# Kernel optimization log

Measured on AMD Instinct MI355X. Metric: run time of the kernel, lower is better.

## Reference

```python
import jax, jax.numpy as jnp
import numpy as np
from jax import lax

VOCAB, EMBED, HIDDEN, LAYERS = 32000, 256, 384, 6
B, S = 16, 512
SCALE = 0.05  # keep tanh out of saturation

def setup_inputs() -> dict:
    key = jax.random.key(0)
    ks = jax.random.split(key, 10)
    return {
        "x": jax.random.randint(ks[0], (B, S), 0, VOCAB),
        "emb": jax.random.normal(ks[1], (VOCAB, EMBED), jnp.float32) * SCALE,
        "W_ih0": jax.random.normal(ks[2], (HIDDEN, EMBED), jnp.float32) * SCALE,
        "W_ih": jax.random.normal(ks[3], (LAYERS - 1, HIDDEN, HIDDEN), jnp.float32) * SCALE,
        "W_hh": jax.random.normal(ks[4], (LAYERS, HIDDEN, HIDDEN), jnp.float32) * SCALE,
        "b_ih": jax.random.normal(ks[5], (LAYERS, HIDDEN), jnp.float32) * SCALE,
        "b_hh": jax.random.normal(ks[6], (LAYERS, HIDDEN), jnp.float32) * SCALE,
        "W_out": jax.random.normal(ks[7], (VOCAB, HIDDEN), jnp.float32) * SCALE,
        "b_out": jax.random.normal(ks[8], (VOCAB,), jnp.float32) * SCALE,
    }

def _rnn_layer(seq, Wi, Wh, bi, bh):
    # seq: [S, B, in_dim]; Elman: h_t = tanh(x_t Wi^T + bi + h_{t-1} Wh^T + bh)
    pre = jnp.einsum('sbi,hi->sbh', seq, Wi) + bi  # batched input projection
    h0 = jnp.zeros((seq.shape[1], Wh.shape[0]), seq.dtype)
    def step(h, p):
        h = jnp.tanh(p + h @ Wh.T + bh)
        return h, h
    _, out = lax.scan(step, h0, pre)
    return out  # [S, B, H]

def reference(x, emb, W_ih0, W_ih, W_hh, b_ih, b_hh, W_out, b_out):
    seq = jnp.swapaxes(emb[x], 0, 1)  # [S, B, E]
    for l in range(LAYERS):
        Wi = W_ih0 if l == 0 else W_ih[l - 1]
        seq = _rnn_layer(seq, Wi, W_hh[l], b_ih[l], b_hh[l])
        # inter-layer dropout: identity in eval mode
    out = jnp.swapaxes(seq, 0, 1)  # [B, S, H]
    return out @ W_out.T + b_out  # [B, S, V]
```

## Files before the change

kernel.cpp:

```cpp
#include <hip/hip_runtime.h>

typedef _Float16 f16;
typedef _Float16 f16x8 __attribute__((ext_vector_type(8)));
typedef _Float16 f16x4 __attribute__((ext_vector_type(4)));
typedef float f32x4 __attribute__((ext_vector_type(4)));

#define MFMA16(a, b, c) __builtin_amdgcn_mfma_f32_16x16x32_f16(a, b, c, 0, 0, 0)

#define CH 16
#define NCH 32
#define SLOT_H (CH * 24 * 64 * 4)

__device__ __forceinline__ float fast_tanh(float x) {
    float e = __builtin_amdgcn_exp2f(x * 2.885390081777927f);
    return 1.0f - 2.0f * __builtin_amdgcn_rcpf(e + 1.0f);
}

__device__ __forceinline__ void lds_barrier() {
    asm volatile("s_waitcnt lgkmcnt(0)" ::: "memory");
    __builtin_amdgcn_s_barrier();
    __builtin_amdgcn_sched_barrier(0);
}

__device__ __forceinline__ f16x8 ld_llc(const f16* p) {
    f16x8 v;
    asm volatile("global_load_dwordx4 %0, %1, off sc0 sc1" : "=v"(v) : "v"(p) : "memory");
    return v;
}
__device__ __forceinline__ f16x4 ld_llc_f16x4(const f16* p) {
    f16x4 v;
    asm volatile("global_load_dwordx2 %0, %1, off sc0 sc1" : "=v"(v) : "v"(p) : "memory");
    return v;
}

#define VWAIT4(N, x0, x1, x2, x3) \
    asm volatile("s_waitcnt vmcnt(" #N ")" : "+v"(x0), "+v"(x1), "+v"(x2), "+v"(x3))
#define VWAITH6(N, p0, p1, p2, p3, p4, p5) \
    asm volatile("s_waitcnt vmcnt(" #N ")" : "+v"(p0), "+v"(p1), "+v"(p2), "+v"(p3), "+v"(p4), "+v"(p5))

__device__ __forceinline__ void wait_flag(const int* f, int target) {
    if (threadIdx.x == 0) {
        while (__hip_atomic_load(f, __ATOMIC_RELAXED, __HIP_MEMORY_SCOPE_AGENT) < target) {
            __builtin_amdgcn_s_sleep(1);
        }
    }
    __syncthreads();
}
__device__ __forceinline__ void set_flag(int* f, int val) {
    __syncthreads();
    if (threadIdx.x == 0)
        __hip_atomic_store(f, val, __ATOMIC_RELEASE, __HIP_MEMORY_SCOPE_AGENT);
}

__global__ void cvt_kernel(const float* __restrict__ src, f16* __restrict__ dst, const int n4) {
    const int i = blockIdx.x * blockDim.x + threadIdx.x;
    if (i < n4) {
        const float4 v = ((const float4*)src)[i];
        f16x4 o = { (f16)v.x, (f16)v.y, (f16)v.z, (f16)v.w };
        *(f16x4*)(dst + (size_t)i * 4) = o;
    }
}

__global__ void bias_combine_kernel(const float* __restrict__ b_ih, const float* __restrict__ b_hh,
                                    float* __restrict__ bias_c) {
    const int i = blockIdx.x * blockDim.x + threadIdx.x;
    if (i < 6 * 384) bias_c[i] = b_ih[i] + b_hh[i];
}

__global__ void embed_kernel(const int* __restrict__ x, const float* __restrict__ emb,
                             f16* __restrict__ seq0) {
    const int token = blockIdx.x;
    const int s = token >> 4, b = token & 15;
    const int idx = x[b * 512 + s];
    const float4 v = ((const float4*)(emb + (size_t)idx * 256))[threadIdx.x];
    f16x4 o = { (f16)v.x, (f16)v.y, (f16)v.z, (f16)v.w };
    *(f16x4*)(seq0 + (size_t)token * 256 + threadIdx.x * 4) = o;
}

template<int NK>
__device__ __forceinline__ void a_role(const f16* __restrict__ in_seq,
                                       const f16* __restrict__ Wi,
                                       const float* __restrict__ bias,
                                       f16* __restrict__ preL,
                                       const int* flag_in, int* flag_pre, const int* flag_seq,
                                       const int L) {
    const int tid = threadIdx.x, lane = tid & 63, w = tid >> 6;
    const int lr = lane & 15, lq = lane >> 4;
    const int KIN = NK * 32;

    f16x8 WiF[6][NK];
#pragma unroll
    for (int i = 0; i < 6; ++i) {
        const f16* wrow = Wi + (size_t)((w * 6 + i) * 16 + lr) * KIN + lq * 8;
#pragma unroll
        for (int kk = 0; kk < NK; ++kk) WiF[i][kk] = *(const f16x8*)(wrow + kk * 32);
    }
    float bv[6];
#pragma unroll
    for (int i = 0; i < 6; ++i) bv[i] = bias[(w * 6 + i) * 16 + lr];

    for (int c = 0; c < NCH; ++c) {
        if (L > 0) wait_flag(flag_in, c + 1);
        if (c >= 4) wait_flag(flag_seq, c - 3);

        f16* slot = preL + (size_t)(c & 3) * SLOT_H;
#pragma unroll 1
        for (int sc = 0; sc < CH; ++sc) {
            const int t = c * CH + sc;
            f32x4 acc[6];
#pragma unroll
            for (int i = 0; i < 6; ++i) acc[i] = (f32x4){ bv[i], bv[i], bv[i], bv[i] };

            const f16* ar = in_seq + (size_t)(t * 16 + lr) * KIN + lq * 8;
            f16x8 a[NK];
#pragma unroll
            for (int kk = 0; kk < NK; ++kk) a[kk] = ld_llc(ar + kk * 32);
            if constexpr (NK == 12) {
                VWAIT4(8, a[0], a[1], a[2], a[3]);
#pragma unroll
                for (int kk = 0; kk < 4; ++kk)
#pragma unroll
                    for (int i = 0; i < 6; ++i) acc[i] = MFMA16(a[kk], WiF[i][kk], acc[i]);
                VWAIT4(4, a[4], a[5], a[6], a[7]);
#pragma unroll
                for (int kk = 4; kk < 8; ++kk)
#pragma unroll
                    for (int i = 0; i < 6; ++i) acc[i] = MFMA16(a[kk], WiF[i][kk], acc[i]);
                VWAIT4(0, a[8], a[9], a[10], a[11]);
#pragma unroll
                for (int kk = 8; kk < 12; ++kk)
#pragma unroll
                    for (int i = 0; i < 6; ++i) acc[i] = MFMA16(a[kk], WiF[i][kk], acc[i]);
            } else {
                VWAIT4(4, a[0], a[1], a[2], a[3]);
#pragma unroll
                for (int kk = 0; kk < 4; ++kk)
#pragma unroll
                    for (int i = 0; i < 6; ++i) acc[i] = MFMA16(a[kk], WiF[i][kk], acc[i]);
                VWAIT4(0, a[4], a[5], a[6], a[7]);
#pragma unroll
                for (int kk = 4; kk < 8; ++kk)
#pragma unroll
                    for (int i = 0; i < 6; ++i) acc[i] = MFMA16(a[kk], WiF[i][kk], acc[i]);
            }
#pragma unroll
            for (int i = 0; i < 6; ++i) {
                f16x4 ph = { (f16)acc[i][0], (f16)acc[i][1], (f16)acc[i][2], (f16)acc[i][3] };
                *(f16x4*)(slot + ((size_t)(sc * 24 + w * 6 + i) * 64 + lane) * 4) = ph;
            }
        }
        set_flag(flag_pre, c + 1);
    }
}

__device__ __forceinline__ void b_role(const f16* __restrict__ preL,
                                       const f16* __restrict__ Wh,
                                       f16* __restrict__ out_seq,
                                       const int* flag_pre, int* flag_seq,
                                       f16 (*hbuf)[16][392]) {
    const int tid = threadIdx.x, lane = tid & 63, w = tid >> 6;
    const int lr = lane & 15, lq = lane >> 4, kb = lq * 8;

    for (int i = tid; i < 2 * 16 * 392; i += 256) (&hbuf[0][0][0])[i] = (f16)0.0f;

    f16x8 WhF[6][12];
#pragma unroll
    for (int i = 0; i < 6; ++i) {
        const f16* wrow = Wh + (size_t)((w * 6 + i) * 16 + lr) * 384 + kb;
#pragma unroll
        for (int kk = 0; kk < 12; ++kk) WhF[i][kk] = *(const f16x8*)(wrow + kk * 32);
    }
    __syncthreads();

    const int crow = tid >> 4;
    const int ccol = (tid & 15) * 8;

    for (int c = 0; c < NCH; ++c) {
        wait_flag(flag_pre, c + 1);
        const f16* slot = preL + (size_t)(c & 3) * SLOT_H;

#pragma unroll 1
        for (int g = 0; g < CH / 4; ++g) {
            f16x4 pr[4][6];
#pragma unroll
            for (int s = 0; s < 4; ++s)
#pragma unroll
                for (int i = 0; i < 6; ++i)
                    pr[s][i] = ld_llc_f16x4(slot + ((size_t)((g * 4 + s) * 24 + w * 6 + i) * 64 + lane) * 4);
            VWAITH6(0, pr[0][0], pr[0][1], pr[0][2], pr[0][3], pr[0][4], pr[0][5]);
            VWAITH6(0, pr[1][0], pr[1][1], pr[1][2], pr[1][3], pr[1][4], pr[1][5]);
            VWAITH6(0, pr[2][0], pr[2][1], pr[2][2], pr[2][3], pr[2][4], pr[2][5]);
            VWAITH6(0, pr[3][0], pr[3][1], pr[3][2], pr[3][3], pr[3][4], pr[3][5]);

#pragma unroll
            for (int s4 = 0; s4 < 4; ++s4) {
                const int sc = g * 4 + s4;
                const int t = c * CH + sc;
                f32x4 acc[6];
#pragma unroll
                for (int i = 0; i < 6; ++i) acc[i] = (f32x4){ 0.f, 0.f, 0.f, 0.f };

                const f16* hb = &hbuf[sc & 1][0][0] + lr * 392 + kb;
#pragma unroll
                for (int kk = 0; kk < 12; ++kk) {
                    const f16x8 a = *(const f16x8*)(hb + kk * 32);
#pragma unroll
                    for (int i = 0; i < 6; ++i) acc[i] = MFMA16(a, WhF[i][kk], acc[i]);
                }

                f16* hn = &hbuf[(sc + 1) & 1][0][0];
#pragma unroll
                for (int i = 0; i < 6; ++i) {
                    const int n = (w * 6 + i) * 16 + lr;
#pragma unroll
                    for (int r = 0; r < 4; ++r) {
                        const float v = acc[i][r] + (float)pr[s4][i][r];
                        hn[(lq * 4 + r) * 392 + n] = (f16)fast_tanh(v);
                    }
                }
                lds_barrier();
                const f16* hs = &hbuf[(sc + 1) & 1][0][0] + crow * 392 + ccol;
                f16* og = out_seq + (size_t)(t * 16 + crow) * 384 + ccol;
#pragma unroll
                for (int p = 0; p < 3; ++p)
                    *(f16x8*)(og + p * 128) = *(const f16x8*)(hs + p * 128);
            }
        }
        set_flag(flag_seq, c + 1);
    }
}

__global__ __launch_bounds__(256, 1) void pipeline_kernel(
    const f16* __restrict__ seq0, const f16* __restrict__ Wi0,
    const f16* __restrict__ WiR, const f16* __restrict__ WhAll,
    const float* __restrict__ biasAll, f16* __restrict__ sA, f16* __restrict__ sB,
    f16* __restrict__ preRing, int* __restrict__ flags) {
    __shared__ f16 hbuf[2][16][392];
    const int bid = blockIdx.x;
    if (bid < 6) {
        const int L = bid;
        const f16* in_seq = (L == 0) ? seq0 : ((L & 1) ? sA : sB);
        const f16* Wi = (L == 0) ? Wi0 : (WiR + (size_t)(L - 1) * 384 * 384);
        f16* preL = preRing + (size_t)L * 4 * SLOT_H;
        if (L == 0)
            a_role<8>(in_seq, Wi, biasAll, preL, nullptr, flags + 8, flags + 0, 0);
        else
            a_role<12>(in_seq, Wi, biasAll + L * 384, preL, flags + (L - 1), flags + 8 + L, flags + L, L);
    } else {
        const int L = bid - 6;
        f16* outb = (L & 1) ? sB : sA;
        b_role(preRing + (size_t)L * 4 * SLOT_H, WhAll + (size_t)L * 384 * 384, outb,
               flags + 8 + L, flags + L, hbuf);
    }
}

__global__ __launch_bounds__(256) void out_proj_kernel(
    const f16* __restrict__ A, const f16* __restrict__ Bm,
    const float* __restrict__ bias, float* __restrict__ C) {
    __shared__ f16 As[128][40];
    __shared__ f16 Bs[128][40];
    const int tid = threadIdx.x, lane = tid & 63, w = tid >> 6;
    const int lr = lane & 15, lq = lane >> 4;
    const int lin = blockIdx.x;
    const int swz = (lin & 7) * 2000 + (lin >> 3);
    const int bn = swz >> 6;
    const int bm = swz & 63;
    const int wm = w >> 1, wn = w & 1;

    f32x4 acc[4][4];
#pragma unroll
    for (int i = 0; i < 4; ++i)
#pragma unroll
        for (int j = 0; j < 4; ++j) acc[i][j] = (f32x4){ 0.f, 0.f, 0.f, 0.f };

    const int sr = tid >> 1, sh = tid & 1;
    const f16* Ag = A + (size_t)(bm * 128 + sr) * 384 + sh * 16;
    const f16* Bg = Bm + (size_t)(bn * 128 + sr) * 384 + sh * 16;

    for (int kt = 0; kt < 12; ++kt) {
        const f16x8 a0 = *(const f16x8*)(Ag + kt * 32);
        const f16x8 a1 = *(const f16x8*)(Ag + kt * 32 + 8);
        const f16x8 b0 = *(const f16x8*)(Bg + kt * 32);
        const f16x8 b1 = *(const f16x8*)(Bg + kt * 32 + 8);
        *(f16x8*)(&As[sr][sh * 16]) = a0;
        *(f16x8*)(&As[sr][sh * 16 + 8]) = a1;
        *(f16x8*)(&Bs[sr][sh * 16]) = b0;
        *(f16x8*)(&Bs[sr][sh * 16 + 8]) = b1;
        __syncthreads();
        f16x8 af[4], bf[4];
#pragma unroll
        for (int mi = 0; mi < 4; ++mi) af[mi] = *(const f16x8*)(&As[wm * 64 + mi * 16 + lr][lq * 8]);
#pragma unroll
        for (int ni = 0; ni < 4; ++ni) bf[ni] = *(const f16x8*)(&Bs[wn * 64 + ni * 16 + lr][lq * 8]);
#pragma unroll
        for (int mi = 0; mi < 4; ++mi)
#pragma unroll
            for (int ni = 0; ni < 4; ++ni) acc[mi][ni] = MFMA16(af[mi], bf[ni], acc[mi][ni]);
        __syncthreads();
    }

    float bv[4];
#pragma unroll
    for (int ni = 0; ni < 4; ++ni) bv[ni] = bias[bn * 128 + wn * 64 + ni * 16 + lr];
#pragma unroll
    for (int mi = 0; mi < 4; ++mi) {
#pragma unroll
        for (int rr = 0; rr < 4; ++rr) {
            const int m = bm * 128 + wm * 64 + mi * 16 + lq * 4 + rr;
            const int s = m >> 4, b = m & 15;
            float* crow = C + (size_t)(b * 512 + s) * 32000;
#pragma unroll
            for (int ni = 0; ni < 4; ++ni) {
                const int n = bn * 128 + wn * 64 + ni * 16 + lr;
                crow[n] = acc[mi][ni][rr] + bv[ni];
            }
        }
    }
}

extern "C" void kernel_launch(void* const* d_in, const int* in_sizes, int n_in,
                              void* d_out, int out_size, void* d_ws, size_t ws_size,
                              hipStream_t stream) {
    const int* x = (const int*)d_in[0];
    const float* emb = (const float*)d_in[1];
    const float* W_ih0 = (const float*)d_in[2];
    const float* W_ih = (const float*)d_in[3];
    const float* W_hh = (const float*)d_in[4];
    const float* b_ih = (const float*)d_in[5];
    const float* b_hh = (const float*)d_in[6];
    const float* W_out = (const float*)d_in[7];
    const float* b_out = (const float*)d_in[8];
    float* out = (float*)d_out;

    char* ws = (char*)d_ws;
    f16* Wi0_h = (f16*)(ws + 0);
    f16* Wi_h = (f16*)(ws + 196608);
    f16* Wh_h = (f16*)(ws + 1671168);
    f16* Wout_h = (f16*)(ws + 3440640);
    float* bias_c = (float*)(ws + 28016640);
    f16* seq0 = (f16*)(ws + 28025856);
    f16* sA = (f16*)(ws + 32220160);
    f16* sB = (f16*)(ws + 38511616);
    f16* preRing = (f16*)(ws + 44803072);
    int* flags = (int*)(ws + 49521664);
    if (ws_size < 49521920u) return;

    hipMemsetAsync(flags, 0, 256, stream);
    cvt_kernel<<<96, 256, 0, stream>>>(W_ih0, Wi0_h, 24576);
    cvt_kernel<<<720, 256, 0, stream>>>(W_ih, Wi_h, 184320);
    cvt_kernel<<<864, 256, 0, stream>>>(W_hh, Wh_h, 221184);
    cvt_kernel<<<12000, 256, 0, stream>>>(W_out, Wout_h, 3072000);
    bias_combine_kernel<<<9, 256, 0, stream>>>(b_ih, b_hh, bias_c);
    embed_kernel<<<8192, 64, 0, stream>>>(x, emb, seq0);

    pipeline_kernel<<<12, 256, 0, stream>>>(seq0, Wi0_h, Wi_h, Wh_h, bias_c,
                                            sA, sB, preRing, flags);

    out_proj_kernel<<<16000, 256, 0, stream>>>(sB, Wout_h, b_out, out);
}
```

Baseline: 1.806 ms.

## Double-buffer LDS in output projection and vectorize stores via transposed MFMA

The output projection GEMM now uses two LDS buffers and prefetches the next K tile's global loads into registers while the current tile is computed, which removes one barrier per iteration. The MFMA operands are swapped so each lane holds four consecutive columns, letting the epilogue write 16-byte float4 stores and load the bias as a vector. This targets the large 16x512x32000 fp32 output write and global load latency. In exchange it doubles LDS use, adds register pressure from the prefetch, and forces the loop to stay rolled.

```diff
diff --git a/kernel.cpp b/kernel.cpp
--- a/kernel.cpp
+++ b/kernel.cpp
@@ -257,8 +257,8 @@
 __global__ __launch_bounds__(256) void out_proj_kernel(
     const f16* __restrict__ A, const f16* __restrict__ Bm,
     const float* __restrict__ bias, float* __restrict__ C) {
-    __shared__ f16 As[128][40];
-    __shared__ f16 Bs[128][40];
+    __shared__ f16 As[2][128][40];
+    __shared__ f16 Bs[2][128][40];
     const int tid = threadIdx.x, lane = tid & 63, w = tid >> 6;
     const int lr = lane & 15, lq = lane >> 4;
     const int lin = blockIdx.x;
@@ -277,43 +277,51 @@
     const f16* Ag = A + (size_t)(bm * 128 + sr) * 384 + sh * 16;
     const f16* Bg = Bm + (size_t)(bn * 128 + sr) * 384 + sh * 16;
 
+    f16x8 a0 = *(const f16x8*)(Ag);
+    f16x8 a1 = *(const f16x8*)(Ag + 8);
+    f16x8 b0 = *(const f16x8*)(Bg);
+    f16x8 b1 = *(const f16x8*)(Bg + 8);
+
+#pragma unroll 1
     for (int kt = 0; kt < 12; ++kt) {
-        const f16x8 a0 = *(const f16x8*)(Ag + kt * 32);
-        const f16x8 a1 = *(const f16x8*)(Ag + kt * 32 + 8);
-        const f16x8 b0 = *(const f16x8*)(Bg + kt * 32);
-        const f16x8 b1 = *(const f16x8*)(Bg + kt * 32 + 8);
-        *(f16x8*)(&As[sr][sh * 16]) = a0;
-        *(f16x8*)(&As[sr][sh * 16 + 8]) = a1;
-        *(f16x8*)(&Bs[sr][sh * 16]) = b0;
-        *(f16x8*)(&Bs[sr][sh * 16 + 8]) = b1;
+        const int cur = kt & 1;
+        *(f16x8*)(&As[cur][sr][sh * 16]) = a0;
+        *(f16x8*)(&As[cur][sr][sh * 16 + 8]) = a1;
+        *(f16x8*)(&Bs[cur][sr][sh * 16]) = b0;
+        *(f16x8*)(&Bs[cur][sr][sh * 16 + 8]) = b1;
+        if (kt < 11) {
+            a0 = *(const f16x8*)(Ag + (kt + 1) * 32);
+            a1 = *(const f16x8*)(Ag + (kt + 1) * 32 + 8);
+            b0 = *(const f16x8*)(Bg + (kt + 1) * 32);
+            b1 = *(const f16x8*)(Bg + (kt + 1) * 32 + 8);
+        }
         __syncthreads();
         f16x8 af[4], bf[4];
 #pragma unroll
-        for (int mi = 0; mi < 4; ++mi) af[mi] = *(const f16x8*)(&As[wm * 64 + mi * 16 + lr][lq * 8]);
-#pragma unroll
-        for (int ni = 0; ni < 4; ++ni) bf[ni] = *(const f16x8*)(&Bs[wn * 64 + ni * 16 + lr][lq * 8]);
+        for (int mi = 0; mi < 4; ++mi) af[mi] = *(const f16x8*)(&As[cur][wm * 64 + mi * 16 + lr][lq * 8]);
+#pragma unroll
+        for (int ni = 0; ni < 4; ++ni) bf[ni] = *(const f16x8*)(&Bs[cur][wn * 64 + ni * 16 + lr][lq * 8]);
 #pragma unroll
         for (int mi = 0; mi < 4; ++mi)
 #pragma unroll
-            for (int ni = 0; ni < 4; ++ni) acc[mi][ni] = MFMA16(af[mi], bf[ni], acc[mi][ni]);
-        __syncthreads();
-    }
-
-    float bv[4];
-#pragma unroll
-    for (int ni = 0; ni < 4; ++ni) bv[ni] = bias[bn * 128 + wn * 64 + ni * 16 + lr];
+            for (int ni = 0; ni < 4; ++ni)
+                acc[mi][ni] = MFMA16(bf[ni], af[mi], acc[mi][ni]);
+    }
+
+    f32x4 bvv[4];
+#pragma unroll
+    for (int ni = 0; ni < 4; ++ni)
+        bvv[ni] = *(const f32x4*)(bias + bn * 128 + wn * 64 + ni * 16 + lq * 4);
 #pragma unroll
     for (int mi = 0; mi < 4; ++mi) {
-#pragma unroll
-        for (int rr = 0; rr < 4; ++rr) {
-            const int m = bm * 128 + wm * 64 + mi * 16 + lq * 4 + rr;
-            const int s = m >> 4, b = m & 15;
-            float* crow = C + (size_t)(b * 512 + s) * 32000;
-#pragma unroll
-            for (int ni = 0; ni < 4; ++ni) {
-                const int n = bn * 128 + wn * 64 + ni * 16 + lr;
-                crow[n] = acc[mi][ni][rr] + bv[ni];
-            }
+        const int m = bm * 128 + wm * 64 + mi * 16 + lr;
+        const int s = m >> 4, b = m & 15;
+        float* crow = C + (size_t)(b * 512 + s) * 32000;
+#pragma unroll
+        for (int ni = 0; ni < 4; ++ni) {
+            const int n = bn * 128 + wn * 64 + ni * 16 + lq * 4;
+            f32x4 o = acc[mi][ni] + bvv[ni];
+            *(f32x4*)(crow + n) = o;
         }
     }
 }
```

Measured after the change: 1.760 ms. -2.5%, faster.
